# Kernel optimization log

Hardware: AMD Instinct MI355X
Metric: run time of the kernel (lower is better)

Reference implementation:

```python
import jax, jax.numpy as jnp
import numpy as np

EMBED = 256
HEADS = 8
HEAD_DIM = EMBED // HEADS  # 32, even for RoPE
INIT_VAL = 1.0
HEADS_RANGE = 3.0


def rotate_every_two(x):
    # (x1, x2) -> (-x2, x1) on interleaved pairs of last dim
    x1 = x[..., ::2]
    x2 = x[..., 1::2]
    return jnp.stack([-x2, x1], axis=-1).reshape(x.shape)


def theta_shift(x, sin, cos):
    # x: [B, heads, H, W, D]; sin/cos: [H, W, D] broadcast over B, heads
    return x * cos + rotate_every_two(x) * sin


def rel_pos_2d(H, W):
    # RetNetRelPos2d: RoPE angles + per-head exponential decay mask
    angle = 1.0 / (10000.0 ** jnp.linspace(0.0, 1.0, HEAD_DIM // 2))
    angle = jnp.repeat(angle, 2)  # [D]
    idx = jnp.arange(H * W, dtype=jnp.float32)
    sin = jnp.sin(idx[:, None] * angle[None, :]).reshape(H, W, HEAD_DIM)
    cos = jnp.cos(idx[:, None] * angle[None, :]).reshape(H, W, HEAD_DIM)
    h_idx = jnp.arange(HEADS, dtype=jnp.float32)
    decay = jnp.log(1.0 - 2.0 ** (-INIT_VAL - HEADS_RANGE * h_idx / HEADS))  # [heads]
    gh, gw = jnp.meshgrid(jnp.arange(H), jnp.arange(W), indexing='ij')
    grid = jnp.stack([gh, gw], axis=-1).reshape(H * W, 2)  # [N,2]
    dist = jnp.abs(grid[:, None, :] - grid[None, :, :]).sum(-1)  # [N,N] L1 distance
    mask = dist[None, :, :].astype(jnp.float32) * decay[:, None, None]  # [heads,N,N]
    return sin, cos, mask


def setup_inputs() -> dict:
    key = jax.random.key(0)
    ks = jax.random.split(key, 8)
    B, H, W, C = 2, 48, 48, EMBED
    s = 0.02
    return {
        'x': jax.random.normal(ks[0], (B, H, W, C), jnp.float32),
        'Wq': jax.random.normal(ks[1], (C, C), jnp.float32) * s,
        'bq': jnp.zeros((C,), jnp.float32),
        'Wk': jax.random.normal(ks[2], (C, C), jnp.float32) * s,
        'bk': jnp.zeros((C,), jnp.float32),
        'Wv': jax.random.normal(ks[3], (C, C), jnp.float32) * s,
        'bv': jnp.zeros((C,), jnp.float32),
        'lepe_w': jax.random.normal(ks[4], (C, 1, 5, 5), jnp.float32) * s,  # depthwise 5x5
        'lepe_b': jnp.zeros((C,), jnp.float32),
        'Wo': jax.random.normal(ks[5], (C, C), jnp.float32) * s,
        'bo': jnp.zeros((C,), jnp.float32),
    }


def reference(x, Wq, bq, Wk, bk, Wv, bv, lepe_w, lepe_b, Wo, bo):
    B, H, W, C = x.shape
    N = H * W
    sin, cos, mask = rel_pos_2d(H, W)
    scaling = HEAD_DIM ** -0.5

    q = x @ Wq + bq
    k = (x @ Wk + bk) * scaling
    v = x @ Wv + bv

    # lepe: depthwise 5x5 conv on v (BHWC)
    lepe = jax.lax.conv_general_dilated(
        v.transpose(0, 3, 1, 2), lepe_w, (1, 1), 'SAME',
        feature_group_count=C, dimension_numbers=('NCHW', 'OIHW', 'NCHW'))
    lepe = lepe.transpose(0, 2, 3, 1) + lepe_b  # [B,H,W,C]

    def split_heads(t):
        return t.reshape(B, H, W, HEADS, HEAD_DIM).transpose(0, 3, 1, 2, 4)

    qr = theta_shift(split_heads(q), sin, cos).reshape(B, HEADS, N, HEAD_DIM)
    kr = theta_shift(split_heads(k), sin, cos).reshape(B, HEADS, N, HEAD_DIM)
    vv = split_heads(v).reshape(B, HEADS, N, HEAD_DIM)

    attn = jnp.einsum('bhnd,bhmd->bhnm', qr, kr) + mask[None]  # [B,heads,N,N]
    attn = jax.nn.softmax(attn, axis=-1)
    out = jnp.einsum('bhnm,bhmd->bhnd', attn, vv)
    out = out.transpose(0, 2, 1, 3).reshape(B, H, W, C)
    out = out + lepe
    return out @ Wo + bo
```

## Files before the change

### kernel.cpp

```cpp
#include <hip/hip_runtime.h>
#include <hip/hip_bf16.h>
#include <math.h>

#define NN 2304
#define ROWSZ 4608
#define SZ (ROWSZ*256)

typedef __attribute__((ext_vector_type(8))) short short8;
typedef __attribute__((ext_vector_type(4))) float f32x4;

__device__ __forceinline__ float bf2f(unsigned short u) {
    return __uint_as_float(((unsigned int)u) << 16);
}
__device__ __forceinline__ unsigned short f2bf(float f) {
    unsigned int u = __float_as_uint(f);
    u += 0x7FFFu + ((u >> 16) & 1u);
    return (unsigned short)(u >> 16);
}
__device__ __forceinline__ unsigned int pack_bf2(float a, float b) {
    return (unsigned int)f2bf(a) | ((unsigned int)f2bf(b) << 16);
}

__device__ __forceinline__ float ub2f(unsigned int v, int r) {
#if defined(__has_builtin)
#if __has_builtin(__builtin_amdgcn_cvt_f32_ubyte0)
    switch (r) {
        case 0: return __builtin_amdgcn_cvt_f32_ubyte0(v);
        case 1: return __builtin_amdgcn_cvt_f32_ubyte1(v);
        case 2: return __builtin_amdgcn_cvt_f32_ubyte2(v);
        default: return __builtin_amdgcn_cvt_f32_ubyte3(v);
    }
#else
    return (float)((v >> (8*r)) & 0xFFu);
#endif
#else
    return (float)((v >> (8*r)) & 0xFFu);
#endif
}

template<int F32>
__device__ __forceinline__ float ldin(const void* p, int i) {
    if constexpr (F32) return ((const float*)p)[i];
    else return bf2f(((const unsigned short*)p)[i]);
}

__global__ void detect_kernel(const unsigned int* __restrict__ x, int* __restrict__ flag) {
    int t = threadIdx.x;
    int cnt = 0;
    for (int i = t; i < 256; i += 64) {
        unsigned int e = (x[i] >> 7) & 0xFFu;
        cnt += (e < 87u || e > 167u) ? 1 : 0;
    }
    #pragma unroll
    for (int o = 32; o; o >>= 1) cnt += __shfl_down(cnt, o);
    if (t == 0) *flag = (cnt >= 32) ? 1 : 0;
}

__global__ __launch_bounds__(256) void dist_kernel(unsigned char* __restrict__ D,
                                                   float2* __restrict__ scT) {
    const int nq = blockIdx.x;
    const int yq = (nq*21846) >> 20, xq = nq - yq*48;
    unsigned int* drow = reinterpret_cast<unsigned int*>(D + (size_t)nq*NN);
    for (int idx = threadIdx.x; idx < 576; idx += 256) {
        const int kp0 = idx*4;
        unsigned int wv = 0;
        #pragma unroll
        for (int r = 0; r < 4; ++r) {
            int kp = kp0 + r;
            int yk = (kp*21846) >> 20;
            int xk = kp - yk*48;
            unsigned int dist = __usad((unsigned)yq, (unsigned)yk,
                                __usad((unsigned)xq, (unsigned)xk, 0u));
            wv |= dist << (8*r);
        }
        drow[idx] = wv;
    }
    if (threadIdx.x < 16) {
        const int j = threadIdx.x;
        const float ang = exp2f((float)j * (-0.8858474919699633f));
        float sv, cv;
        sincosf((float)nq * ang, &sv, &cv);
        scT[nq*16 + j] = make_float2(sv, cv);
    }
}

__global__ __launch_bounds__(256) void xprep_kernel(const void* __restrict__ x,
    const int* __restrict__ flag, unsigned short* __restrict__ xb)
{
    const int e = (blockIdx.x*256 + threadIdx.x) * 8;
    if (*flag) {
        const float* xp = (const float*)x + e;
        float4 a0 = *reinterpret_cast<const float4*>(xp);
        float4 a1 = *reinterpret_cast<const float4*>(xp + 4);
        uint4 o;
        o.x = pack_bf2(a0.x, a0.y); o.y = pack_bf2(a0.z, a0.w);
        o.z = pack_bf2(a1.x, a1.y); o.w = pack_bf2(a1.z, a1.w);
        *reinterpret_cast<uint4*>(xb + e) = o;
    } else {
        *reinterpret_cast<uint4*>(xb + e) =
            *reinterpret_cast<const uint4*>((const unsigned short*)x + e);
    }
}

__global__ __launch_bounds__(256) void wprep_kernel(
    const void* __restrict__ Wq, const void* __restrict__ bq,
    const void* __restrict__ Wk, const void* __restrict__ bk,
    const void* __restrict__ Wv, const void* __restrict__ bv,
    const void* __restrict__ Wo, const void* __restrict__ bo,
    const int* __restrict__ flag,
    unsigned short* __restrict__ Wt, float* __restrict__ bb)
{
    __shared__ float wsh[256][17];
    const int t = threadIdx.x;
    const int m = blockIdx.y;
    const int oc0 = blockIdx.x * 16;
    const void* W  = (m == 0) ? Wq : (m == 1) ? Wk : (m == 2) ? Wv : Wo;
    const void* bs = (m == 0) ? bq : (m == 1) ? bk : (m == 2) ? bv : bo;
    const float scale = (m == 1) ? 0.17677669529663687f * 1.4426950408889634f : 1.0f;
    const int F = *flag;
    #pragma unroll
    for (int j2 = 0; j2 < 16; ++j2)
        wsh[t][j2] = F ? ((const float*)W)[t*256 + oc0 + j2]
                       : bf2f(((const unsigned short*)W)[t*256 + oc0 + j2]);
    __syncthreads();
    const int j = t >> 4, seg = t & 15;
    unsigned int u[8];
    #pragma unroll
    for (int i = 0; i < 8; ++i) {
        float v0 = wsh[seg*16 + 2*i][j]     * scale;
        float v1 = wsh[seg*16 + 2*i + 1][j] * scale;
        u[i] = pack_bf2(v0, v1);
    }
    unsigned short* drow = Wt + ((size_t)(m*256 + oc0 + j))*256 + seg*16;
    *reinterpret_cast<uint4*>(drow)     = make_uint4(u[0], u[1], u[2], u[3]);
    *reinterpret_cast<uint4*>(drow + 8) = make_uint4(u[4], u[5], u[6], u[7]);
    if (blockIdx.x == 0)
        bb[m*256 + t] = (F ? ((const float*)bs)[t]
                           : bf2f(((const unsigned short*)bs)[t])) * scale;
}

__global__ __launch_bounds__(256) void qkv_mfma(
    const unsigned short* __restrict__ xb, const unsigned short* __restrict__ Wt,
    const float* __restrict__ bb, const float2* __restrict__ scT,
    unsigned short* __restrict__ q, unsigned short* __restrict__ k,
    unsigned short* __restrict__ v, unsigned short* __restrict__ vT)
{
    __shared__ __align__(16) char smem[43136];
    char* sc_lds = smem + 40960;
    const int t = threadIdx.x;
    const int w = t >> 6, lane = t & 63;
    const int q16 = lane & 15, quad = lane >> 4;
    const int m = blockIdx.y;
    const int tok0 = blockIdx.x * 16;
    const int b = (tok0 >= NN) ? 1 : 0;
    const int n0 = tok0 - b*NN;

    {
        float2 sv = scT[(size_t)(n0 + (t >> 4))*16 + (t & 15)];
        *reinterpret_cast<float2*>(sc_lds + (t >> 4)*136 + (t & 15)*8) = sv;
    }
    short8 af[8];
    #pragma unroll
    for (int kk = 0; kk < 8; ++kk)
        af[kk] = *reinterpret_cast<const short8*>(
            xb + (size_t)(tok0 + q16)*256 + kk*32 + quad*8);

    const unsigned short* Wm = Wt + (size_t)m*256*256;
    {
        const unsigned short* src = Wm + (size_t)t*256;
        #pragma unroll
        for (int s = 0; s < 4; ++s)
            *reinterpret_cast<uint4*>(smem + t*80 + s*16) =
                *reinterpret_cast<const uint4*>(src + s*8);
    }
    __syncthreads();

    f32x4 acc[4];
    #pragma unroll
    for (int tt = 0; tt < 4; ++tt) acc[tt] = (f32x4){0.f, 0.f, 0.f, 0.f};
    int cur = 0;
    for (int kk = 0; kk < 8; ++kk) {
        const int kkn = (kk < 7) ? kk + 1 : 7;
        uint4 nw[4];
        const unsigned short* src = Wm + (size_t)t*256 + kkn*32;
        #pragma unroll
        for (int s = 0; s < 4; ++s) nw[s] = *reinterpret_cast<const uint4*>(src + s*8);
        char* Wl = smem + cur*20480;
        #pragma unroll
        for (int tt = 0; tt < 4; ++tt) {
            short8 bf = *reinterpret_cast<const short8*>(
                Wl + (w*64 + tt*16 + q16)*80 + quad*16);
            acc[tt] = __builtin_amdgcn_mfma_f32_16x16x32_bf16(af[kk], bf, acc[tt], 0, 0, 0);
        }
        char* Wn = smem + (cur ^ 1)*20480;
        #pragma unroll
        for (int s = 0; s < 4; ++s)
            *reinterpret_cast<uint4*>(Wn + t*80 + s*16) = nw[s];
        __syncthreads();
        cur ^= 1;
    }

    char* ostage = smem;
    float bias[4];
    #pragma unroll
    for (int tt = 0; tt < 4; ++tt) bias[tt] = bb[m*256 + w*64 + tt*16 + q16];
    if (m < 2) {
        const int odd = q16 & 1;
        #pragma unroll
        for (int tt = 0; tt < 4; ++tt) {
            const int j = ((tt & 1) << 3) + (q16 >> 1);
            #pragma unroll
            for (int r = 0; r < 4; ++r) {
                const int tokL = quad*4 + r;
                float a = acc[tt][r] + bias[tt];
                float ap = __shfl_xor(a, 1);
                float2 sc = *reinterpret_cast<const float2*>(sc_lds + tokL*136 + j*8);
                float val = odd ? fmaf(a, sc.y, ap*sc.x) : fmaf(a, sc.y, -ap*sc.x);
                *reinterpret_cast<unsigned short*>(
                    ostage + tokL*528 + (w*64 + tt*16 + q16)*2) = f2bf(val);
            }
        }
    } else {
        #pragma unroll
        for (int tt = 0; tt < 4; ++tt) {
            #pragma unroll
            for (int r = 0; r < 4; ++r)
                *reinterpret_cast<unsigned short*>(
                    ostage + (quad*4 + r)*528 + (w*64 + tt*16 + q16)*2)
                    = f2bf(acc[tt][r] + bias[tt]);
        }
    }
    __syncthreads();
    unsigned short* dst = (m == 0) ? q : (m == 1) ? k : v;
    {
        char* p = ostage + (t >> 4)*528 + (t & 15)*32;
        uint4 a0 = *reinterpret_cast<uint4*>(p);
        uint4 a1 = *reinterpret_cast<uint4*>(p + 16);
        unsigned short* drow = dst + (size_t)(tok0 + (t >> 4))*256 + (t & 15)*16;
        *reinterpret_cast<uint4*>(drow)     = a0;
        *reinterpret_cast<uint4*>(drow + 8) = a1;
    }
    if (m == 2) {
        const int h = t >> 5, d = t & 31;
        unsigned int vp[8];
        #pragma unroll
        for (int i = 0; i < 8; ++i) {
            unsigned short e0 = *reinterpret_cast<unsigned short*>(
                ostage + (2*i)*528 + (h*32 + d)*2);
            unsigned short e1 = *reinterpret_cast<unsigned short*>(
                ostage + (2*i + 1)*528 + (h*32 + d)*2);
            vp[i] = (unsigned int)e0 | ((unsigned int)e1 << 16);
        }
        unsigned short* vt = vT + ((size_t)(b*8 + h)*32 + d)*NN + n0;
        *reinterpret_cast<uint4*>(vt)     = make_uint4(vp[0], vp[1], vp[2], vp[3]);
        *reinterpret_cast<uint4*>(vt + 8) = make_uint4(vp[4], vp[5], vp[6], vp[7]);
    }
}

template<int F32>
__device__ __forceinline__ void lepe_body(const unsigned short* __restrict__ v,
    const void* __restrict__ w, const void* __restrict__ wb,
    unsigned short* __restrict__ lepe)
{
    int c = threadIdx.x;
    int pos = blockIdx.x;
    int b  = pos >= NN ? 1 : 0;
    int yx = pos - b*NN;
    int y  = (yx*21846) >> 20;
    int xx = yx - y*48;
    float acc = ldin<F32>(wb, c);
    #pragma unroll
    for (int ky = 0; ky < 5; ++ky) {
        int yy = y + ky - 2;
        if ((unsigned)yy >= 48u) continue;
        #pragma unroll
        for (int kx = 0; kx < 5; ++kx) {
            int xc = xx + kx - 2;
            if ((unsigned)xc >= 48u) continue;
            acc = fmaf(bf2f(v[((b*NN + yy*48 + xc)<<8) + c]), ldin<F32>(w, c*25 + ky*5 + kx), acc);
        }
    }
    lepe[(pos<<8) + c] = f2bf(acc);
}

__global__ __launch_bounds__(256) void lepe_kernel(const unsigned short* __restrict__ v,
    const void* __restrict__ w, const void* __restrict__ wb,
    const int* __restrict__ flag, unsigned short* __restrict__ lepe)
{
    if (*flag) lepe_body<1>(v, w, wb, lepe);
    else       lepe_body<0>(v, w, wb, lepe);
}

template<int DIRECT>
__global__ __launch_bounds__(256) void attn_kernel(
    const unsigned short* __restrict__ q, const unsigned short* __restrict__ k,
    const unsigned short* __restrict__ vT, const unsigned char* __restrict__ D,
    unsigned short* __restrict__ o, float* __restrict__ pacc, float* __restrict__ pl)
{
    __shared__ char smem[27648];
    const int t = threadIdx.x;
    const int w = t >> 6, lane = t & 63;
    const int q16 = lane & 15, quad = lane >> 4;
    char* PsB = smem + 19456 + w*2048;
    const int bh = blockIdx.y, b = bh >> 3, h = bh & 7;
    const int q0 = blockIdx.x*64 + w*16;
    const int nq = q0 + q16;
    const float decay2 = log2f(1.0f - exp2f(-1.0f - 0.375f*(float)h));
    short8 qfrag = *reinterpret_cast<const short8*>(q + ((size_t)(b*NN + nq))*256 + h*32 + quad*8);
    f32x4 acc0 = {0.f,0.f,0.f,0.f}, acc1 = {0.f,0.f,0.f,0.f};
    const f32x4 zero = {0.f,0.f,0.f,0.f};
    float lacc = 0.0f;
    const unsigned short* kbase = k + (size_t)(b*NN)*256 + h*32;
    const unsigned short* vtb = vT + (size_t)bh*32*NN;
    const unsigned char* Dbase = D + (size_t)nq*NN + quad*4;
    const int skr = t >> 2, skp = t & 3;
    const int svd = t >> 3, svp = t & 7;
    const int psW = q16*16 + (quad & 1)*8;
    const int qsh = quad >> 1;
    const int nchunk = 36 / gridDim.z;
    const int kt0 = blockIdx.z * nchunk;

    {
        uint4 kraw = *reinterpret_cast<const uint4*>(kbase + (kt0*64 + skr)*256 + skp*8);
        uint4 vraw = *reinterpret_cast<const uint4*>(vtb + svd*NN + kt0*64 + svp*8);
        *reinterpret_cast<uint4*>(smem + skr*80 + skp*16) = kraw;
        *reinterpret_cast<uint4*>(smem + 5120 + svd*144 + svp*16) = vraw;
    }
    __syncthreads();

    int cur = 0;
    for (int kc = 0; kc < nchunk; ++kc) {
        const int kt = kt0 + kc;
        const int ktn = (kc + 1 < nchunk) ? kt + 1 : kt;
        uint4 nk = *reinterpret_cast<const uint4*>(kbase + (ktn*64 + skr)*256 + skp*8);
        uint4 nv = *reinterpret_cast<const uint4*>(vtb + svd*NN + ktn*64 + svp*8);
        unsigned int dw[4];
        #pragma unroll
        for (int tt = 0; tt < 4; ++tt)
            dw[tt] = *reinterpret_cast<const unsigned int*>(Dbase + kt*64 + tt*16);
        char* KsB = smem + cur*9728;
        char* VtB = KsB + 5120;
        f32x4 st[4];
        #pragma unroll
        for (int tt = 0; tt < 4; ++tt) {
            short8 kf = *reinterpret_cast<const short8*>(KsB + (tt*16 + q16)*80 + quad*16);
            st[tt] = __builtin_amdgcn_mfma_f32_16x16x32_bf16(kf, qfrag, zero, 0, 0, 0);
        }
        unsigned int pk[8];
        float lsum = 0.0f;
        #pragma unroll
        for (int tt = 0; tt < 4; ++tt) {
            float p[4];
            #pragma unroll
            for (int r = 0; r < 4; ++r) {
                p[r] = exp2f(fmaf(decay2, ub2f(dw[tt], r), st[tt][r]));
                lsum += p[r];
            }
            pk[tt*2]   = __builtin_amdgcn_perm(__float_as_uint(p[1]), __float_as_uint(p[0]), 0x07060302);
            pk[tt*2+1] = __builtin_amdgcn_perm(__float_as_uint(p[3]), __float_as_uint(p[2]), 0x07060302);
        }
        lacc += lsum;
        #pragma unroll
        for (int tt = 0; tt < 4; ++tt) {
            uint2 pp; pp.x = pk[tt*2]; pp.y = pk[tt*2+1];
            *reinterpret_cast<uint2*>(PsB + (tt >> 1)*1024 + (((tt*2) + qsh) & 3)*256 + psW) = pp;
        }
        #pragma unroll
        for (int kh = 0; kh < 2; ++kh) {
            short8 pf = *reinterpret_cast<const short8*>(PsB + kh*1024 + lane*16);
            short8 v0 = *reinterpret_cast<const short8*>(VtB + q16*144 + kh*64 + quad*16);
            short8 v1 = *reinterpret_cast<const short8*>(VtB + (16 + q16)*144 + kh*64 + quad*16);
            acc0 = __builtin_amdgcn_mfma_f32_16x16x32_bf16(v0, pf, acc0, 0, 0, 0);
            acc1 = __builtin_amdgcn_mfma_f32_16x16x32_bf16(v1, pf, acc1, 0, 0, 0);
        }
        char* KsN = smem + (cur^1)*9728;
        *reinterpret_cast<uint4*>(KsN + skr*80 + skp*16) = nk;
        *reinterpret_cast<uint4*>(KsN + 5120 + svd*144 + svp*16) = nv;
        __syncthreads();
        cur ^= 1;
    }
    lacc += __shfl_xor(lacc, 16);
    lacc += __shfl_xor(lacc, 32);
    if constexpr (DIRECT) {
        float invl = 1.0f / lacc;
        unsigned short* orow = o + ((size_t)(b*NN + nq))*256 + h*32;
        uint2 w0, w1;
        w0.x = pack_bf2(acc0[0]*invl, acc0[1]*invl);
        w0.y = pack_bf2(acc0[2]*invl, acc0[3]*invl);
        w1.x = pack_bf2(acc1[0]*invl, acc1[1]*invl);
        w1.y = pack_bf2(acc1[2]*invl, acc1[3]*invl);
        *reinterpret_cast<uint2*>(orow + quad*4)      = w0;
        *reinterpret_cast<uint2*>(orow + 16 + quad*4) = w1;
    } else {
        float* pb = pacc + ((size_t)(blockIdx.z*16 + bh)*NN + nq)*32;
        *reinterpret_cast<f32x4*>(pb + quad*4)      = acc0;
        *reinterpret_cast<f32x4*>(pb + 16 + quad*4) = acc1;
        if (quad == 0) pl[((size_t)blockIdx.z*16 + bh)*NN + nq] = lacc;
    }
}

__global__ __launch_bounds__(256) void out_mfma(
    const unsigned short* __restrict__ o,
    const float* __restrict__ pacc, const float* __restrict__ pl,
    const unsigned short* __restrict__ lp,
    const unsigned short* __restrict__ Wt, const float* __restrict__ bb,
    const int* __restrict__ flag, void* __restrict__ out, int nsplit)
{
    __shared__ __align__(16) char smem[49408];
    char* Ast = smem + 40960;
    const int t = threadIdx.x;
    const int w = t >> 6, lane = t & 63;
    const int q16 = lane & 15, quad = lane >> 4;
    const int tok0 = blockIdx.x * 16;

    {
        const int r = t >> 4, c0 = (t & 15) * 16;
        const int nqr = tok0 + r;
        uint4 lb0 = *reinterpret_cast<const uint4*>(lp + (size_t)nqr*256 + c0);
        uint4 lb1 = *reinterpret_cast<const uint4*>(lp + (size_t)nqr*256 + c0 + 8);
        const unsigned short* lu0 = reinterpret_cast<const unsigned short*>(&lb0);
        const unsigned short* lu1 = reinterpret_cast<const unsigned short*>(&lb1);
        float av[16];
        if (nsplit == 0) {
            uint4 oa0 = *reinterpret_cast<const uint4*>(o + (size_t)nqr*256 + c0);
            uint4 oa1 = *reinterpret_cast<const uint4*>(o + (size_t)nqr*256 + c0 + 8);
            const unsigned short* ou0 = reinterpret_cast<const unsigned short*>(&oa0);
            const unsigned short* ou1 = reinterpret_cast<const unsigned short*>(&oa1);
            #pragma unroll
            for (int j = 0; j < 8; ++j) {
                av[j]     = bf2f(ou0[j]) + bf2f(lu0[j]);
                av[8 + j] = bf2f(ou1[j]) + bf2f(lu1[j]);
            }
        } else {
            const int b = nqr >= NN ? 1 : 0;
            const int nq = nqr - b*NN;
            const int bh = b*8 + (c0 >> 5);
            const int d0 = c0 & 31;
            float s[16];
            #pragma unroll
            for (int j = 0; j < 16; ++j) s[j] = 0.f;
            float lsum = 0.f;
            for (int p = 0; p < nsplit; ++p) {
                const float* pb = pacc + ((size_t)(p*16 + bh)*NN + nq)*32 + d0;
                #pragma unroll
                for (int j4 = 0; j4 < 4; ++j4) {
                    f32x4 vv = *reinterpret_cast<const f32x4*>(pb + j4*4);
                    s[j4*4+0] += vv[0]; s[j4*4+1] += vv[1];
                    s[j4*4+2] += vv[2]; s[j4*4+3] += vv[3];
                }
                lsum += pl[((size_t)p*16 + bh)*NN + nq];
            }
            float invl = 1.0f / lsum;
            #pragma unroll
            for (int j = 0; j < 8; ++j) {
                av[j]     = fmaf(s[j],     invl, bf2f(lu0[j]));
                av[8 + j] = fmaf(s[8 + j], invl, bf2f(lu1[j]));
            }
        }
        unsigned int u[8];
        #pragma unroll
        for (int i = 0; i < 8; ++i) u[i] = pack_bf2(av[2*i], av[2*i+1]);
        *reinterpret_cast<uint4*>(Ast + r*528 + c0*2)      = make_uint4(u[0],u[1],u[2],u[3]);
        *reinterpret_cast<uint4*>(Ast + r*528 + c0*2 + 16) = make_uint4(u[4],u[5],u[6],u[7]);
    }
    const unsigned short* Wm = Wt + (size_t)3*256*256;
    {
        const unsigned short* src = Wm + (size_t)t*256;
        #pragma unroll
        for (int s2 = 0; s2 < 4; ++s2)
            *reinterpret_cast<uint4*>(smem + t*80 + s2*16) =
                *reinterpret_cast<const uint4*>(src + s2*8);
    }
    __syncthreads();
    short8 af[8];
    #pragma unroll
    for (int kk = 0; kk < 8; ++kk)
        af[kk] = *reinterpret_cast<const short8*>(Ast + q16*528 + kk*64 + quad*16);

    f32x4 acc[4];
    #pragma unroll
    for (int tt = 0; tt < 4; ++tt) acc[tt] = (f32x4){0.f, 0.f, 0.f, 0.f};
    int cur = 0;
    for (int kk = 0; kk < 8; ++kk) {
        const int kkn = (kk < 7) ? kk + 1 : 7;
        uint4 nw[4];
        const unsigned short* src = Wm + (size_t)t*256 + kkn*32;
        #pragma unroll
        for (int s2 = 0; s2 < 4; ++s2) nw[s2] = *reinterpret_cast<const uint4*>(src + s2*8);
        char* Wl = smem + cur*20480;
        #pragma unroll
        for (int tt = 0; tt < 4; ++tt) {
            short8 bf = *reinterpret_cast<const short8*>(
                Wl + (w*64 + tt*16 + q16)*80 + quad*16);
            acc[tt] = __builtin_amdgcn_mfma_f32_16x16x32_bf16(af[kk], bf, acc[tt], 0, 0, 0);
        }
        char* Wn = smem + (cur ^ 1)*20480;
        #pragma unroll
        for (int s2 = 0; s2 < 4; ++s2)
            *reinterpret_cast<uint4*>(Wn + t*80 + s2*16) = nw[s2];
        __syncthreads();
        cur ^= 1;
    }
    const int F = *flag;
    float bias[4];
    #pragma unroll
    for (int tt = 0; tt < 4; ++tt) bias[tt] = bb[3*256 + w*64 + tt*16 + q16];
    if (F) {
        char* ostf = smem;
        #pragma unroll
        for (int tt = 0; tt < 4; ++tt) {
            #pragma unroll
            for (int r = 0; r < 4; ++r)
                *reinterpret_cast<float*>(ostf + (quad*4 + r)*1040
                    + (w*64 + tt*16 + q16)*4) = acc[tt][r] + bias[tt];
        }
        __syncthreads();
        char* p = ostf + (t >> 4)*1040 + (t & 15)*64;
        float4 x0 = *reinterpret_cast<float4*>(p);
        float4 x1 = *reinterpret_cast<float4*>(p + 16);
        float4 x2 = *reinterpret_cast<float4*>(p + 32);
        float4 x3 = *reinterpret_cast<float4*>(p + 48);
        float* drow = (float*)out + (size_t)(tok0 + (t >> 4))*256 + (t & 15)*16;
        *reinterpret_cast<float4*>(drow)      = x0;
        *reinterpret_cast<float4*>(drow + 4)  = x1;
        *reinterpret_cast<float4*>(drow + 8)  = x2;
        *reinterpret_cast<float4*>(drow + 12) = x3;
    } else {
        char* ost = smem;
        #pragma unroll
        for (int tt = 0; tt < 4; ++tt) {
            #pragma unroll
            for (int r = 0; r < 4; ++r)
                *reinterpret_cast<unsigned short*>(ost + (quad*4 + r)*528
                    + (w*64 + tt*16 + q16)*2) = f2bf(acc[tt][r] + bias[tt]);
        }
        __syncthreads();
        char* p = ost + (t >> 4)*528 + (t & 15)*32;
        uint4 a0 = *reinterpret_cast<uint4*>(p);
        uint4 a1 = *reinterpret_cast<uint4*>(p + 16);
        unsigned short* drow = (unsigned short*)out + (size_t)(tok0 + (t >> 4))*256 + (t & 15)*16;
        *reinterpret_cast<uint4*>(drow)     = a0;
        *reinterpret_cast<uint4*>(drow + 8) = a1;
    }
}

extern "C" void kernel_launch(void* const* d_in, const int* in_sizes, int n_in,
                              void* d_out, int out_size, void* d_ws, size_t ws_size,
                              hipStream_t stream)
{
    const void* x  = d_in[0];
    const void* Wq = d_in[1];
    const void* bq = d_in[2];
    const void* Wk = d_in[3];
    const void* bk = d_in[4];
    const void* Wv = d_in[5];
    const void* bv = d_in[6];
    const void* lw = d_in[7];
    const void* lb = d_in[8];
    const void* Wo = d_in[9];
    const void* bo = d_in[10];

    int* flag = (int*)d_ws;
    unsigned short* qb   = (unsigned short*)((char*)d_ws + 256);
    unsigned short* kbuf = qb   + (size_t)SZ;
    unsigned short* vbuf = kbuf + (size_t)SZ;
    unsigned short* obuf = vbuf + (size_t)SZ;
    unsigned short* lbuf = obuf + (size_t)SZ;
    unsigned short* vtb  = lbuf + (size_t)SZ;
    unsigned char*  Dtab = (unsigned char*)(vtb + (size_t)SZ);
    float2* scT = (float2*)(Dtab + (size_t)NN*NN);
    unsigned short* xb = (unsigned short*)(scT + (size_t)NN*16);
    unsigned short* Wt = xb + (size_t)SZ;
    float* bb = (float*)(Wt + (size_t)4*256*256);

    const size_t base = 256 + 6*(size_t)SZ*2 + (size_t)NN*NN
                      + (size_t)NN*16*8 + (size_t)SZ*2
                      + (size_t)4*256*256*2 + (size_t)4*256*4;
    const size_t per_split = (size_t)16*NN*32*4 + (size_t)16*NN*4;
    int nsplit = 0;
    if      (ws_size >= base + 4*per_split) nsplit = 4;
    else if (ws_size >= base + 2*per_split) nsplit = 2;
    else if (ws_size >= base + 1*per_split) nsplit = 1;
    float* pacc = (float*)((char*)d_ws + base);
    float* pl   = pacc + (size_t)(nsplit ? nsplit : 1)*16*NN*32;

    detect_kernel<<<1, 64, 0, stream>>>((const unsigned int*)x, flag);
    dist_kernel<<<NN, 256, 0, stream>>>(Dtab, scT);
    xprep_kernel<<<576, 256, 0, stream>>>(x, flag, xb);
    wprep_kernel<<<dim3(16,4), 256, 0, stream>>>(Wq, bq, Wk, bk, Wv, bv, Wo, bo, flag, Wt, bb);
    qkv_mfma<<<dim3(288,3), 256, 0, stream>>>(xb, Wt, bb, scT, qb, kbuf, vbuf, vtb);
    lepe_kernel<<<4608, 256, 0, stream>>>(vbuf, lw, lb, flag, lbuf);
    if (nsplit) {
        attn_kernel<0><<<dim3(36, 16, nsplit), 256, 0, stream>>>(qb, kbuf, vtb, Dtab, obuf, pacc, pl);
    } else {
        attn_kernel<1><<<dim3(36, 16, 1), 256, 0, stream>>>(qb, kbuf, vtb, Dtab, obuf, pacc, pl);
    }
    out_mfma<<<288, 256, 0, stream>>>(obuf, pacc, pl, lbuf, Wt, bb, flag, d_out, nsplit);
}
```

Measured before the change: 214.8 us.

## Load K/V MFMA fragments directly from global into registers, dropping LDS staging

The attention kernel no longer stages K and V^T tiles through double-buffered shared memory with block-wide barriers. Each wave loads its MFMA operand fragments straight from global memory into registers, prefetching the next tile one iteration ahead. Shared memory shrinks to the per-wave P scratch, which removes the __syncthreads and may raise occupancy. The cost is that all four waves now fetch the same K/V data redundantly through cache, and the K rows are loaded with a 512-byte stride, giving less coalesced access and more register pressure.

```diff
diff --git a/kernel.cpp b/kernel.cpp
--- a/kernel.cpp
+++ b/kernel.cpp
@@ -297,11 +297,11 @@
     const unsigned short* __restrict__ vT, const unsigned char* __restrict__ D,
     unsigned short* __restrict__ o, float* __restrict__ pacc, float* __restrict__ pl)
 {
-    __shared__ char smem[27648];
+    __shared__ char smem[8192];
     const int t = threadIdx.x;
     const int w = t >> 6, lane = t & 63;
     const int q16 = lane & 15, quad = lane >> 4;
-    char* PsB = smem + 19456 + w*2048;
+    char* PsB = smem + w*2048;
     const int bh = blockIdx.y, b = bh >> 3, h = bh & 7;
     const int q0 = blockIdx.x*64 + w*16;
     const int nq = q0 + q16;
@@ -310,42 +310,48 @@
     f32x4 acc0 = {0.f,0.f,0.f,0.f}, acc1 = {0.f,0.f,0.f,0.f};
     const f32x4 zero = {0.f,0.f,0.f,0.f};
     float lacc = 0.0f;
-    const unsigned short* kbase = k + (size_t)(b*NN)*256 + h*32;
-    const unsigned short* vtb = vT + (size_t)bh*32*NN;
+    const unsigned short* kptr  = k  + (size_t)(b*NN)*256 + h*32 + (size_t)q16*256 + quad*8;
+    const unsigned short* vptr0 = vT + (size_t)bh*32*NN + (size_t)q16*NN + quad*8;
+    const unsigned short* vptr1 = vptr0 + (size_t)16*NN;
     const unsigned char* Dbase = D + (size_t)nq*NN + quad*4;
-    const int skr = t >> 2, skp = t & 3;
-    const int svd = t >> 3, svp = t & 7;
     const int psW = q16*16 + (quad & 1)*8;
     const int qsh = quad >> 1;
     const int nchunk = 36 / gridDim.z;
     const int kt0 = blockIdx.z * nchunk;
-
-    {
-        uint4 kraw = *reinterpret_cast<const uint4*>(kbase + (kt0*64 + skr)*256 + skp*8);
-        uint4 vraw = *reinterpret_cast<const uint4*>(vtb + svd*NN + kt0*64 + svp*8);
-        *reinterpret_cast<uint4*>(smem + skr*80 + skp*16) = kraw;
-        *reinterpret_cast<uint4*>(smem + 5120 + svd*144 + svp*16) = vraw;
-    }
-    __syncthreads();
-
-    int cur = 0;
+    const int ktL = kt0 + nchunk - 1;
+
+    short8 kf[4], vf[4];
+    unsigned int dw[4];
+    #pragma unroll
+    for (int tt = 0; tt < 4; ++tt) {
+        kf[tt] = *reinterpret_cast<const short8*>(kptr + (kt0*64 + tt*16)*256);
+        dw[tt] = *reinterpret_cast<const unsigned int*>(Dbase + kt0*64 + tt*16);
+    }
+    #pragma unroll
+    for (int kh = 0; kh < 2; ++kh) {
+        vf[kh*2]   = *reinterpret_cast<const short8*>(vptr0 + kt0*64 + kh*32);
+        vf[kh*2+1] = *reinterpret_cast<const short8*>(vptr1 + kt0*64 + kh*32);
+    }
+
     for (int kc = 0; kc < nchunk; ++kc) {
         const int kt = kt0 + kc;
-        const int ktn = (kc + 1 < nchunk) ? kt + 1 : kt;
-        uint4 nk = *reinterpret_cast<const uint4*>(kbase + (ktn*64 + skr)*256 + skp*8);
-        uint4 nv = *reinterpret_cast<const uint4*>(vtb + svd*NN + ktn*64 + svp*8);
-        unsigned int dw[4];
+        const int ktn = (kt < ktL) ? kt + 1 : ktL;
+        short8 nkf[4], nvf[4];
+        unsigned int ndw[4];
+        #pragma unroll
+        for (int tt = 0; tt < 4; ++tt) {
+            nkf[tt] = *reinterpret_cast<const short8*>(kptr + (ktn*64 + tt*16)*256);
+            ndw[tt] = *reinterpret_cast<const unsigned int*>(Dbase + ktn*64 + tt*16);
+        }
+        #pragma unroll
+        for (int kh = 0; kh < 2; ++kh) {
+            nvf[kh*2]   = *reinterpret_cast<const short8*>(vptr0 + ktn*64 + kh*32);
+            nvf[kh*2+1] = *reinterpret_cast<const short8*>(vptr1 + ktn*64 + kh*32);
+        }
+        f32x4 st[4];
         #pragma unroll
         for (int tt = 0; tt < 4; ++tt)
-            dw[tt] = *reinterpret_cast<const unsigned int*>(Dbase + kt*64 + tt*16);
-        char* KsB = smem + cur*9728;
-        char* VtB = KsB + 5120;
-        f32x4 st[4];
-        #pragma unroll
-        for (int tt = 0; tt < 4; ++tt) {
-            short8 kf = *reinterpret_cast<const short8*>(KsB + (tt*16 + q16)*80 + quad*16);
-            st[tt] = __builtin_amdgcn_mfma_f32_16x16x32_bf16(kf, qfrag, zero, 0, 0, 0);
-        }
+            st[tt] = __builtin_amdgcn_mfma_f32_16x16x32_bf16(kf[tt], qfrag, zero, 0, 0, 0);
         unsigned int pk[8];
         float lsum = 0.0f;
         #pragma unroll
@@ -368,16 +374,11 @@
         #pragma unroll
         for (int kh = 0; kh < 2; ++kh) {
             short8 pf = *reinterpret_cast<const short8*>(PsB + kh*1024 + lane*16);
-            short8 v0 = *reinterpret_cast<const short8*>(VtB + q16*144 + kh*64 + quad*16);
-            short8 v1 = *reinterpret_cast<const short8*>(VtB + (16 + q16)*144 + kh*64 + quad*16);
-            acc0 = __builtin_amdgcn_mfma_f32_16x16x32_bf16(v0, pf, acc0, 0, 0, 0);
-            acc1 = __builtin_amdgcn_mfma_f32_16x16x32_bf16(v1, pf, acc1, 0, 0, 0);
-        }
-        char* KsN = smem + (cur^1)*9728;
-        *reinterpret_cast<uint4*>(KsN + skr*80 + skp*16) = nk;
-        *reinterpret_cast<uint4*>(KsN + 5120 + svd*144 + svp*16) = nv;
-        __syncthreads();
-        cur ^= 1;
+            acc0 = __builtin_amdgcn_mfma_f32_16x16x32_bf16(vf[kh*2],   pf, acc0, 0, 0, 0);
+            acc1 = __builtin_amdgcn_mfma_f32_16x16x32_bf16(vf[kh*2+1], pf, acc1, 0, 0, 0);
+        }
+        #pragma unroll
+        for (int i = 0; i < 4; ++i) { kf[i] = nkf[i]; vf[i] = nvf[i]; dw[i] = ndw[i]; }
     }
     lacc += __shfl_xor(lacc, 16);
     lacc += __shfl_xor(lacc, 32);
```

New measurement: 284.8 us. +32.6%, slower.

## Process two query tiles per wave in attention and pre-transpose lepe weights

Applied to the files above, without the earlier changes.

Each attention wave now handles 32 queries instead of 16, so every K fragment and V fragment loaded from shared memory feeds two sets of MFMAs. The grid x-dimension is halved to match. Separately, the depthwise conv weights are converted to fp32 and transposed once in wprep, giving lepe coalesced weight loads and no flag-dependent dtype branch. The trade-off is higher register and LDS use per block and half as many blocks, which may lower occupancy.

```diff
diff --git a/kernel.cpp b/kernel.cpp
--- a/kernel.cpp
+++ b/kernel.cpp
@@ -107,17 +107,32 @@
     const void* __restrict__ Wk, const void* __restrict__ bk,
     const void* __restrict__ Wv, const void* __restrict__ bv,
     const void* __restrict__ Wo, const void* __restrict__ bo,
+    const void* __restrict__ lw, const void* __restrict__ lb,
     const int* __restrict__ flag,
-    unsigned short* __restrict__ Wt, float* __restrict__ bb)
+    unsigned short* __restrict__ Wt, float* __restrict__ bb,
+    float* __restrict__ lwT)
 {
     __shared__ float wsh[256][17];
     const int t = threadIdx.x;
     const int m = blockIdx.y;
+    const int F = *flag;
+    if (m == 4) {
+        if (blockIdx.x != 0) return;
+        float wv[25];
+        #pragma unroll
+        for (int j = 0; j < 25; ++j)
+            wv[j] = F ? ((const float*)lw)[t*25 + j]
+                      : bf2f(((const unsigned short*)lw)[t*25 + j]);
+        #pragma unroll
+        for (int j = 0; j < 25; ++j) lwT[j*256 + t] = wv[j];
+        bb[4*256 + t] = F ? ((const float*)lb)[t]
+                          : bf2f(((const unsigned short*)lb)[t]);
+        return;
+    }
     const int oc0 = blockIdx.x * 16;
     const void* W  = (m == 0) ? Wq : (m == 1) ? Wk : (m == 2) ? Wv : Wo;
     const void* bs = (m == 0) ? bq : (m == 1) ? bk : (m == 2) ? bv : bo;
     const float scale = (m == 1) ? 0.17677669529663687f * 1.4426950408889634f : 1.0f;
-    const int F = *flag;
     #pragma unroll
     for (int j2 = 0; j2 < 16; ++j2)
         wsh[t][j2] = F ? ((const float*)W)[t*256 + oc0 + j2]
@@ -257,9 +272,8 @@
     }
 }
 
-template<int F32>
-__device__ __forceinline__ void lepe_body(const unsigned short* __restrict__ v,
-    const void* __restrict__ w, const void* __restrict__ wb,
+__global__ __launch_bounds__(256) void lepe_kernel(const unsigned short* __restrict__ v,
+    const float* __restrict__ lwT, const float* __restrict__ bb,
     unsigned short* __restrict__ lepe)
 {
     int c = threadIdx.x;
@@ -268,7 +282,7 @@
     int yx = pos - b*NN;
     int y  = (yx*21846) >> 20;
     int xx = yx - y*48;
-    float acc = ldin<F32>(wb, c);
+    float acc = bb[4*256 + c];
     #pragma unroll
     for (int ky = 0; ky < 5; ++ky) {
         int yy = y + ky - 2;
@@ -277,18 +291,11 @@
         for (int kx = 0; kx < 5; ++kx) {
             int xc = xx + kx - 2;
             if ((unsigned)xc >= 48u) continue;
-            acc = fmaf(bf2f(v[((b*NN + yy*48 + xc)<<8) + c]), ldin<F32>(w, c*25 + ky*5 + kx), acc);
+            acc = fmaf(bf2f(v[((b*NN + yy*48 + xc)<<8) + c]),
+                       lwT[(ky*5 + kx)*256 + c], acc);
         }
     }
     lepe[(pos<<8) + c] = f2bf(acc);
-}
-
-__global__ __launch_bounds__(256) void lepe_kernel(const unsigned short* __restrict__ v,
-    const void* __restrict__ w, const void* __restrict__ wb,
-    const int* __restrict__ flag, unsigned short* __restrict__ lepe)
-{
-    if (*flag) lepe_body<1>(v, w, wb, lepe);
-    else       lepe_body<0>(v, w, wb, lepe);
 }
 
 template<int DIRECT>
@@ -297,22 +304,26 @@
     const unsigned short* __restrict__ vT, const unsigned char* __restrict__ D,
     unsigned short* __restrict__ o, float* __restrict__ pacc, float* __restrict__ pl)
 {
-    __shared__ char smem[27648];
+    __shared__ char smem[35840];
     const int t = threadIdx.x;
     const int w = t >> 6, lane = t & 63;
     const int q16 = lane & 15, quad = lane >> 4;
-    char* PsB = smem + 19456 + w*2048;
+    char* PsW = smem + 19456 + w*4096;
     const int bh = blockIdx.y, b = bh >> 3, h = bh & 7;
-    const int q0 = blockIdx.x*64 + w*16;
-    const int nq = q0 + q16;
+    const int q0 = blockIdx.x*128 + w*32;
+    const int nqA = q0 + q16;
+    const int nqB = nqA + 16;
     const float decay2 = log2f(1.0f - exp2f(-1.0f - 0.375f*(float)h));
-    short8 qfrag = *reinterpret_cast<const short8*>(q + ((size_t)(b*NN + nq))*256 + h*32 + quad*8);
-    f32x4 acc0 = {0.f,0.f,0.f,0.f}, acc1 = {0.f,0.f,0.f,0.f};
+    short8 qfragA = *reinterpret_cast<const short8*>(q + ((size_t)(b*NN + nqA))*256 + h*32 + quad*8);
+    short8 qfragB = *reinterpret_cast<const short8*>(q + ((size_t)(b*NN + nqB))*256 + h*32 + quad*8);
+    f32x4 accA0 = {0.f,0.f,0.f,0.f}, accA1 = {0.f,0.f,0.f,0.f};
+    f32x4 accB0 = {0.f,0.f,0.f,0.f}, accB1 = {0.f,0.f,0.f,0.f};
     const f32x4 zero = {0.f,0.f,0.f,0.f};
-    float lacc = 0.0f;
+    float laccA = 0.0f, laccB = 0.0f;
     const unsigned short* kbase = k + (size_t)(b*NN)*256 + h*32;
     const unsigned short* vtb = vT + (size_t)bh*32*NN;
-    const unsigned char* Dbase = D + (size_t)nq*NN + quad*4;
+    const unsigned char* DbA = D + (size_t)nqA*NN + quad*4;
+    const unsigned char* DbB = D + (size_t)nqB*NN + quad*4;
     const int skr = t >> 2, skp = t & 3;
     const int svd = t >> 3, svp = t & 7;
     const int psW = q16*16 + (quad & 1)*8;
@@ -334,44 +345,78 @@
         const int ktn = (kc + 1 < nchunk) ? kt + 1 : kt;
         uint4 nk = *reinterpret_cast<const uint4*>(kbase + (ktn*64 + skr)*256 + skp*8);
         uint4 nv = *reinterpret_cast<const uint4*>(vtb + svd*NN + ktn*64 + svp*8);
-        unsigned int dw[4];
-        #pragma unroll
-        for (int tt = 0; tt < 4; ++tt)
-            dw[tt] = *reinterpret_cast<const unsigned int*>(Dbase + kt*64 + tt*16);
+        unsigned int dwA[4], dwB[4];
+        #pragma unroll
+        for (int tt = 0; tt < 4; ++tt) {
+            dwA[tt] = *reinterpret_cast<const unsigned int*>(DbA + kt*64 + tt*16);
+            dwB[tt] = *reinterpret_cast<const unsigned int*>(DbB + kt*64 + tt*16);
+        }
         char* KsB = smem + cur*9728;
         char* VtB = KsB + 5120;
-        f32x4 st[4];
-        #pragma unroll
-        for (int tt = 0; tt < 4; ++tt) {
-            short8 kf = *reinterpret_cast<const short8*>(KsB + (tt*16 + q16)*80 + quad*16);
-            st[tt] = __builtin_amdgcn_mfma_f32_16x16x32_bf16(kf, qfrag, zero, 0, 0, 0);
-        }
-        unsigned int pk[8];
-        float lsum = 0.0f;
-        #pragma unroll
-        for (int tt = 0; tt < 4; ++tt) {
-            float p[4];
-            #pragma unroll
-            for (int r = 0; r < 4; ++r) {
-                p[r] = exp2f(fmaf(decay2, ub2f(dw[tt], r), st[tt][r]));
-                lsum += p[r];
-            }
-            pk[tt*2]   = __builtin_amdgcn_perm(__float_as_uint(p[1]), __float_as_uint(p[0]), 0x07060302);
-            pk[tt*2+1] = __builtin_amdgcn_perm(__float_as_uint(p[3]), __float_as_uint(p[2]), 0x07060302);
-        }
-        lacc += lsum;
-        #pragma unroll
-        for (int tt = 0; tt < 4; ++tt) {
-            uint2 pp; pp.x = pk[tt*2]; pp.y = pk[tt*2+1];
-            *reinterpret_cast<uint2*>(PsB + (tt >> 1)*1024 + (((tt*2) + qsh) & 3)*256 + psW) = pp;
+        short8 kf[4];
+        #pragma unroll
+        for (int tt = 0; tt < 4; ++tt)
+            kf[tt] = *reinterpret_cast<const short8*>(KsB + (tt*16 + q16)*80 + quad*16);
+        {
+            f32x4 st[4];
+            #pragma unroll
+            for (int tt = 0; tt < 4; ++tt)
+                st[tt] = __builtin_amdgcn_mfma_f32_16x16x32_bf16(kf[tt], qfragA, zero, 0, 0, 0);
+            unsigned int pk[8];
+            float lsum = 0.0f;
+            #pragma unroll
+            for (int tt = 0; tt < 4; ++tt) {
+                float p[4];
+                #pragma unroll
+                for (int r = 0; r < 4; ++r) {
+                    p[r] = exp2f(fmaf(decay2, ub2f(dwA[tt], r), st[tt][r]));
+                    lsum += p[r];
+                }
+                pk[tt*2]   = __builtin_amdgcn_perm(__float_as_uint(p[1]), __float_as_uint(p[0]), 0x07060302);
+                pk[tt*2+1] = __builtin_amdgcn_perm(__float_as_uint(p[3]), __float_as_uint(p[2]), 0x07060302);
+            }
+            laccA += lsum;
+            #pragma unroll
+            for (int tt = 0; tt < 4; ++tt) {
+                uint2 pp; pp.x = pk[tt*2]; pp.y = pk[tt*2+1];
+                *reinterpret_cast<uint2*>(PsW + (tt >> 1)*1024 + (((tt*2) + qsh) & 3)*256 + psW) = pp;
+            }
+        }
+        {
+            f32x4 st[4];
+            #pragma unroll
+            for (int tt = 0; tt < 4; ++tt)
+                st[tt] = __builtin_amdgcn_mfma_f32_16x16x32_bf16(kf[tt], qfragB, zero, 0, 0, 0);
+            unsigned int pk[8];
+            float lsum = 0.0f;
+            #pragma unroll
+            for (int tt = 0; tt < 4; ++tt) {
+                float p[4];
+                #pragma unroll
+                for (int r = 0; r < 4; ++r) {
+                    p[r] = exp2f(fmaf(decay2, ub2f(dwB[tt], r), st[tt][r]));
+                    lsum += p[r];
+                }
+                pk[tt*2]   = __builtin_amdgcn_perm(__float_as_uint(p[1]), __float_as_uint(p[0]), 0x07060302);
+                pk[tt*2+1] = __builtin_amdgcn_perm(__float_as_uint(p[3]), __float_as_uint(p[2]), 0x07060302);
+            }
+            laccB += lsum;
+            #pragma unroll
+            for (int tt = 0; tt < 4; ++tt) {
+                uint2 pp; pp.x = pk[tt*2]; pp.y = pk[tt*2+1];
+                *reinterpret_cast<uint2*>(PsW + 2048 + (tt >> 1)*1024 + (((tt*2) + qsh) & 3)*256 + psW) = pp;
+            }
         }
         #pragma unroll
         for (int kh = 0; kh < 2; ++kh) {
-            short8 pf = *reinterpret_cast<const short8*>(PsB + kh*1024 + lane*16);
             short8 v0 = *reinterpret_cast<const short8*>(VtB + q16*144 + kh*64 + quad*16);
             short8 v1 = *reinterpret_cast<const short8*>(VtB + (16 + q16)*144 + kh*64 + quad*16);
-            acc0 = __builtin_amdgcn_mfma_f32_16x16x32_bf16(v0, pf, acc0, 0, 0, 0);
-            acc1 = __builtin_amdgcn_mfma_f32_16x16x32_bf16(v1, pf, acc1, 0, 0, 0);
+            short8 pfA = *reinterpret_cast<const short8*>(PsW + kh*1024 + lane*16);
+            short8 pfB = *reinterpret_cast<const short8*>(PsW + 2048 + kh*1024 + lane*16);
+            accA0 = __builtin_amdgcn_mfma_f32_16x16x32_bf16(v0, pfA, accA0, 0, 0, 0);
+            accA1 = __builtin_amdgcn_mfma_f32_16x16x32_bf16(v1, pfA, accA1, 0, 0, 0);
+            accB0 = __builtin_amdgcn_mfma_f32_16x16x32_bf16(v0, pfB, accB0, 0, 0, 0);
+            accB1 = __builtin_amdgcn_mfma_f32_16x16x32_bf16(v1, pfB, accB1, 0, 0, 0);
         }
         char* KsN = smem + (cur^1)*9728;
         *reinterpret_cast<uint4*>(KsN + skr*80 + skp*16) = nk;
@@ -379,23 +424,38 @@
         __syncthreads();
         cur ^= 1;
     }
-    lacc += __shfl_xor(lacc, 16);
-    lacc += __shfl_xor(lacc, 32);
+    laccA += __shfl_xor(laccA, 16);
+    laccA += __shfl_xor(laccA, 32);
+    laccB += __shfl_xor(laccB, 16);
+    laccB += __shfl_xor(laccB, 32);
     if constexpr (DIRECT) {
-        float invl = 1.0f / lacc;
-        unsigned short* orow = o + ((size_t)(b*NN + nq))*256 + h*32;
+        float invA = 1.0f / laccA, invB = 1.0f / laccB;
+        unsigned short* orowA = o + ((size_t)(b*NN + nqA))*256 + h*32;
+        unsigned short* orowB = o + ((size_t)(b*NN + nqB))*256 + h*32;
         uint2 w0, w1;
-        w0.x = pack_bf2(acc0[0]*invl, acc0[1]*invl);
-        w0.y = pack_bf2(acc0[2]*invl, acc0[3]*invl);
-        w1.x = pack_bf2(acc1[0]*invl, acc1[1]*invl);
-        w1.y = pack_bf2(acc1[2]*invl, acc1[3]*invl);
-        *reinterpret_cast<uint2*>(orow + quad*4)      = w0;
-        *reinterpret_cast<uint2*>(orow + 16 + quad*4) = w1;
+        w0.x = pack_bf2(accA0[0]*invA, accA0[1]*invA);
+        w0.y = pack_bf2(accA0[2]*invA, accA0[3]*invA);
+        w1.x = pack_bf2(accA1[0]*invA, accA1[1]*invA);
+        w1.y = pack_bf2(accA1[2]*invA, accA1[3]*invA);
+        *reinterpret_cast<uint2*>(orowA + quad*4)      = w0;
+        *reinterpret_cast<uint2*>(orowA + 16 + quad*4) = w1;
+        w0.x = pack_bf2(accB0[0]*invB, accB0[1]*invB);
+        w0.y = pack_bf2(accB0[2]*invB, accB0[3]*invB);
+        w1.x = pack_bf2(accB1[0]*invB, accB1[1]*invB);
+        w1.y = pack_bf2(accB1[2]*invB, accB1[3]*invB);
+        *reinterpret_cast<uint2*>(orowB + quad*4)      = w0;
+        *reinterpret_cast<uint2*>(orowB + 16 + quad*4) = w1;
     } else {
-        float* pb = pacc + ((size_t)(blockIdx.z*16 + bh)*NN + nq)*32;
-        *reinterpret_cast<f32x4*>(pb + quad*4)      = acc0;
-        *reinterpret_cast<f32x4*>(pb + 16 + quad*4) = acc1;
-        if (quad == 0) pl[((size_t)blockIdx.z*16 + bh)*NN + nq] = lacc;
+        float* pbA = pacc + ((size_t)(blockIdx.z*16 + bh)*NN + nqA)*32;
+        float* pbB = pacc + ((size_t)(blockIdx.z*16 + bh)*NN + nqB)*32;
+        *reinterpret_cast<f32x4*>(pbA + quad*4)      = accA0;
+        *reinterpret_cast<f32x4*>(pbA + 16 + quad*4) = accA1;
+        *reinterpret_cast<f32x4*>(pbB + quad*4)      = accB0;
+        *reinterpret_cast<f32x4*>(pbB + 16 + quad*4) = accB1;
+        if (quad == 0) {
+            pl[((size_t)blockIdx.z*16 + bh)*NN + nqA] = laccA;
+            pl[((size_t)blockIdx.z*16 + bh)*NN + nqB] = laccB;
+        }
     }
 }
 
@@ -571,11 +631,12 @@
     float2* scT = (float2*)(Dtab + (size_t)NN*NN);
     unsigned short* xb = (unsigned short*)(scT + (size_t)NN*16);
     unsigned short* Wt = xb + (size_t)SZ;
-    float* bb = (float*)(Wt + (size_t)4*256*256);
+    float* bb  = (float*)(Wt + (size_t)4*256*256);
+    float* lwT = bb + 5*256;
 
     const size_t base = 256 + 6*(size_t)SZ*2 + (size_t)NN*NN
                       + (size_t)NN*16*8 + (size_t)SZ*2
-                      + (size_t)4*256*256*2 + (size_t)4*256*4;
+                      + (size_t)4*256*256*2 + (size_t)5*256*4 + (size_t)25*256*4;
     const size_t per_split = (size_t)16*NN*32*4 + (size_t)16*NN*4;
     int nsplit = 0;
     if      (ws_size >= base + 4*per_split) nsplit = 4;
@@ -587,13 +648,13 @@
     detect_kernel<<<1, 64, 0, stream>>>((const unsigned int*)x, flag);
     dist_kernel<<<NN, 256, 0, stream>>>(Dtab, scT);
     xprep_kernel<<<576, 256, 0, stream>>>(x, flag, xb);
-    wprep_kernel<<<dim3(16,4), 256, 0, stream>>>(Wq, bq, Wk, bk, Wv, bv, Wo, bo, flag, Wt, bb);
+    wprep_kernel<<<dim3(16,5), 256, 0, stream>>>(Wq, bq, Wk, bk, Wv, bv, Wo, bo, lw, lb, flag, Wt, bb, lwT);
     qkv_mfma<<<dim3(288,3), 256, 0, stream>>>(xb, Wt, bb, scT, qb, kbuf, vbuf, vtb);
-    lepe_kernel<<<4608, 256, 0, stream>>>(vbuf, lw, lb, flag, lbuf);
+    lepe_kernel<<<4608, 256, 0, stream>>>(vbuf, lwT, bb, lbuf);
     if (nsplit) {
-        attn_kernel<0><<<dim3(36, 16, nsplit), 256, 0, stream>>>(qb, kbuf, vtb, Dtab, obuf, pacc, pl);
+        attn_kernel<0><<<dim3(18, 16, nsplit), 256, 0, stream>>>(qb, kbuf, vtb, Dtab, obuf, pacc, pl);
     } else {
-        attn_kernel<1><<<dim3(36, 16, 1), 256, 0, stream>>>(qb, kbuf, vtb, Dtab, obuf, pacc, pl);
+        attn_kernel<1><<<dim3(18, 16, 1), 256, 0, stream>>>(qb, kbuf, vtb, Dtab, obuf, pacc, pl);
     }
     out_mfma<<<288, 256, 0, stream>>>(obuf, pacc, pl, lbuf, Wt, bb, flag, d_out, nsplit);
 }
```

After: 210.6 us. About the same (-2.0%).
